# Kernel optimization log

Hardware: AMD Instinct MI355X
Metric: run time of the kernel (lower is better)

Reference implementation:

```python
import jax, jax.numpy as jnp
import numpy as np

NH = 8
QCH = 256
KCH = 256
VCH = 256


def setup_inputs() -> dict:
    key = jax.random.key(0)
    ks = jax.random.split(key, 6)
    B, C, H, W = 8, 512, 28, 28
    return {
        "inputs": jax.random.normal(ks[0], (B, C, H, W), jnp.float32),
        "inputs_st": jax.random.normal(ks[1], (B, C, H, W), jnp.float32),
        "Wq": jax.random.normal(ks[2], (QCH, C), jnp.float32) * 0.02,
        "bq": jnp.zeros((QCH,), jnp.float32),
        "Wkv": jax.random.normal(ks[3], (KCH + VCH, C), jnp.float32) * 0.02,
        "bkv": jnp.zeros((KCH + VCH,), jnp.float32),
        "Wo": jax.random.normal(ks[4], (512, VCH), jnp.float32) * 0.02,
        "bo": jnp.zeros((512,), jnp.float32),
    }


def reference(inputs, inputs_st, Wq, bq, Wkv, bkv, Wo, bo):
    B, C, H, W = inputs.shape
    dkh = KCH // NH  # scale uses k-channels per head, as in source

    # 1x1 conv projections == channel matmuls
    q = jnp.einsum('bchw,oc->bohw', inputs, Wq) + bq[None, :, None, None]
    kv = jnp.einsum('bchw,oc->bohw', inputs_st, Wkv) + bkv[None, :, None, None]
    k, v = kv[:, :KCH], kv[:, KCH:]

    # split heads: (B, Nh, ch//Nh, H, W)
    q = q.reshape(B, NH, QCH // NH, H, W) * (dkh ** -0.5)
    k = k.reshape(B, NH, KCH // NH, H, W)
    v = v.reshape(B, NH, VCH // NH, H, W)

    flat_q = q.reshape(B, NH, QCH // NH, H * W)
    flat_k = k.reshape(B, NH, KCH // NH, H * W)
    flat_v = v.reshape(B, NH, VCH // NH, H * W)

    # logits: (B, Nh, HqWq, HW) = q^T k
    logits = jnp.einsum('bnds,bndt->bnst', flat_q, flat_k)
    # NOTE: source applies softmax over dim=1 (the head axis), not the key axis
    weights = jax.nn.softmax(logits, axis=1)
    # attn_out: (B, Nh, HqWq, dvh)
    attn_out = jnp.einsum('bnst,bndt->bnsd', weights, flat_v)
    # faithful raw reshapes (no transpose), matching torch.reshape semantics
    attn_out = attn_out.reshape(B, NH, VCH // NH, H, W)
    attn_out = attn_out.reshape(B, VCH, H, W)

    out = jnp.einsum('bchw,oc->bohw', attn_out, Wo) + bo[None, :, None, None]
    return out
```

## Files before the change

### kernel.cpp

```cpp
#include <hip/hip_runtime.h>

#define SS 784
#define NQE 1605632

typedef float f32x4 __attribute__((ext_vector_type(4)));
typedef short s16x8 __attribute__((ext_vector_type(8)));

__device__ inline ushort f2bf(float f) {
    union { float f; unsigned u; } v; v.f = f;
    return (ushort)((v.u + 0x7fff + ((v.u >> 16) & 1)) >> 16);
}
__device__ inline float bf2f(ushort h) {
    union { unsigned u; float f; } v; v.u = ((unsigned)h) << 16;
    return v.f;
}
__device__ inline unsigned cvt_pk_bf16(float lo, float hi) {
    unsigned r;
    asm("v_cvt_pk_bf16_f32 %0, %1, %2" : "=v"(r) : "v"(lo), "v"(hi));
    return r;
}

__global__ __launch_bounds__(256) void transpose_cvt2(const float* __restrict__ X0,
                                                      const float* __restrict__ X1,
                                                      ushort* __restrict__ Xt0,
                                                      ushort* __restrict__ Xt1) {
    __shared__ ushort Ts[64][72];
    const int tid = threadIdx.x;
    const int p0 = blockIdx.x * 64, c0 = blockIdx.y * 64;
    const int z  = blockIdx.z;
    const int b  = z & 7;
    const float*  X  = (z < 8) ? X0 : X1;
    ushort*       Xt = (z < 8) ? Xt0 : Xt1;
    const int cr = tid >> 2, ch = (tid & 3) * 16;
    if (p0 + ch < SS) {
        const float* src = X + ((size_t)b * 512 + c0 + cr) * SS + p0 + ch;
        #pragma unroll
        for (int jj = 0; jj < 4; ++jj) {
            float4 v = *(const float4*)(src + jj * 4);
            Ts[ch + jj * 4 + 0][cr] = f2bf(v.x);
            Ts[ch + jj * 4 + 1][cr] = f2bf(v.y);
            Ts[ch + jj * 4 + 2][cr] = f2bf(v.z);
            Ts[ch + jj * 4 + 3][cr] = f2bf(v.w);
        }
    } else {
        #pragma unroll
        for (int j = 0; j < 16; ++j) Ts[ch + j][cr] = 0;
    }
    __syncthreads();
    const int pr = tid >> 2, cc = (tid & 3) * 16;
    if (p0 + pr < SS) {
        ushort* dst = Xt + ((size_t)b * SS + p0 + pr) * 512 + c0 + cc;
        *(s16x8*)dst       = *(const s16x8*)&Ts[pr][cc];
        *(s16x8*)(dst + 8) = *(const s16x8*)&Ts[pr][cc + 8];
    }
}

__global__ __launch_bounds__(256) void gemm_qkv(const ushort* __restrict__ xt_q,
                                                const ushort* __restrict__ xt_kv,
                                                const float* __restrict__ Wq,
                                                const float* __restrict__ bq,
                                                const float* __restrict__ Wkv,
                                                const float* __restrict__ bkv,
                                                ushort* __restrict__ qt,
                                                ushort* __restrict__ kt,
                                                ushort* __restrict__ vv,
                                                float qscale) {
    __shared__ ushort As[128 * 40];
    __shared__ ushort Bs[128 * 40];
    const int id  = blockIdx.x;
    const int b   = id & 7;
    const int sub = id >> 3;
    const int oy  = sub % 6;
    const int p0  = (sub / 6) * 128;
    const int mode = (oy < 2) ? 0 : (oy < 4 ? 1 : 2);
    const ushort* Xt  = (mode == 0) ? xt_q : xt_kv;
    const float* Wg   = (mode == 0) ? Wq : Wkv;
    const float* bias = (mode == 0) ? bq : bkv;
    const int o0w = (mode == 0) ? oy * 128 : (oy - 2) * 128;

    const int tid = threadIdx.x;
    const int lane = tid & 63, wave = tid >> 6;
    const int wm = wave >> 1, wn = wave & 1;
    const int lg = lane >> 4, lm = lane & 15;
    const int srow = tid >> 1, shalf = (tid & 1) * 16;

    const f32x4 Z4 = {0.f, 0.f, 0.f, 0.f};
    const s16x8 Z8 = {0, 0, 0, 0, 0, 0, 0, 0};
    f32x4 acc[4][4];
    #pragma unroll
    for (int m = 0; m < 4; ++m)
        #pragma unroll
        for (int n = 0; n < 4; ++n) acc[m][n] = Z4;

    for (int c0 = 0; c0 < 512; c0 += 32) {
        __syncthreads();
        {
            const float* src = Wg + (size_t)(o0w + srow) * 512 + c0 + shalf;
            ushort tmp[16];
            #pragma unroll
            for (int jj = 0; jj < 4; ++jj) {
                float4 v = *(const float4*)(src + jj * 4);
                tmp[jj * 4 + 0] = f2bf(v.x); tmp[jj * 4 + 1] = f2bf(v.y);
                tmp[jj * 4 + 2] = f2bf(v.z); tmp[jj * 4 + 3] = f2bf(v.w);
            }
            *(s16x8*)&As[srow * 40 + shalf]     = *(s16x8*)&tmp[0];
            *(s16x8*)&As[srow * 40 + shalf + 8] = *(s16x8*)&tmp[8];
        }
        {
            int p = p0 + srow;
            s16x8 v0 = Z8, v1 = Z8;
            if (p < SS) {
                const ushort* src = Xt + ((size_t)b * SS + p) * 512 + c0 + shalf;
                v0 = *(const s16x8*)src;
                v1 = *(const s16x8*)(src + 8);
            }
            *(s16x8*)&Bs[srow * 40 + shalf]     = v0;
            *(s16x8*)&Bs[srow * 40 + shalf + 8] = v1;
        }
        __syncthreads();
        s16x8 af[4], bf[4];
        #pragma unroll
        for (int m = 0; m < 4; ++m) af[m] = *(const s16x8*)&As[(wm * 64 + m * 16 + lm) * 40 + 8 * lg];
        #pragma unroll
        for (int n = 0; n < 4; ++n) bf[n] = *(const s16x8*)&Bs[(wn * 64 + n * 16 + lm) * 40 + 8 * lg];
        #pragma unroll
        for (int m = 0; m < 4; ++m)
            #pragma unroll
            for (int n = 0; n < 4; ++n)
                acc[m][n] = __builtin_amdgcn_mfma_f32_16x16x32_bf16(af[m], bf[n], acc[m][n], 0, 0, 0);
    }

    if (mode < 2) {
        ushort* outT = (mode == 0) ? qt : kt;
        const float scale = (mode == 0) ? qscale : 1.0f;
        #pragma unroll
        for (int m = 0; m < 4; ++m) {
            const int o = o0w + wm * 64 + m * 16 + 4 * lg;
            float bv[4];
            #pragma unroll
            for (int r = 0; r < 4; ++r) bv[r] = bias[o + r];
            #pragma unroll
            for (int n = 0; n < 4; ++n) {
                const int p = p0 + wn * 64 + n * 16 + lm;
                if (p < SS) {
                    ushort4 w;
                    w.x = f2bf((acc[m][n][0] + bv[0]) * scale);
                    w.y = f2bf((acc[m][n][1] + bv[1]) * scale);
                    w.z = f2bf((acc[m][n][2] + bv[2]) * scale);
                    w.w = f2bf((acc[m][n][3] + bv[3]) * scale);
                    *(ushort4*)&outT[((size_t)b * SS + p) * 256 + o] = w;
                }
            }
        }
    } else {
        #pragma unroll
        for (int m = 0; m < 4; ++m) {
            const int ob = o0w + wm * 64 + m * 16 + 4 * lg;
            float bv[4];
            #pragma unroll
            for (int r = 0; r < 4; ++r) bv[r] = bias[ob + r];
            #pragma unroll
            for (int n = 0; n < 4; ++n) {
                const int p = p0 + wn * 64 + n * 16 + lm;
                if (p < SS) {
                    #pragma unroll
                    for (int r = 0; r < 4; ++r) {
                        const int c = ob - 256 + r;
                        vv[((size_t)b * 256 + c) * SS + p] = f2bf(acc[m][n][r] + bv[r]);
                    }
                }
            }
        }
    }
}

#define KROW 280
#define VROW 40
#define PROW 40

__global__ __launch_bounds__(256, 3) void attn_mfma(const ushort* __restrict__ qt,
                                                    const ushort* __restrict__ kt,
                                                    const ushort* __restrict__ vv,
                                                    ushort* __restrict__ pb,
                                                    ushort* __restrict__ p4) {
    __shared__ ushort ks[32 * KROW];
    __shared__ ushort vs[256 * VROW];
    __shared__ ushort pls[4 * 2 * 16 * PROW];
    const int tid  = threadIdx.x;
    const int lane = tid & 63;
    const int wave = tid >> 6;
    const int b     = blockIdx.x;
    const int stile = blockIdx.y / 5;
    const int ts    = blockIdx.y % 5;
    int strip = stile * 4 + wave;
    const bool valid = (strip < 49);
    if (!valid) strip = 48;
    const int s0 = strip * 16;

    const int lg = lane >> 4, lm = lane & 15;
    const s16x8 Z8 = {0, 0, 0, 0, 0, 0, 0, 0};
    const f32x4 Z4 = {0.f, 0.f, 0.f, 0.f};

    s16x8 qf[8];
    const ushort* qbase = qt + ((size_t)b * SS + s0 + lm) * 256 + 8 * lg;
    #pragma unroll
    for (int n = 0; n < 8; ++n) qf[n] = *(const s16x8*)(qbase + n * 32);

    f32x4 oacc[8][2];
    #pragma unroll
    for (int n = 0; n < 8; ++n) { oacc[n][0] = Z4; oacc[n][1] = Z4; }

    const ushort* ktb = kt + (size_t)b * SS * 256;
    const ushort* vb  = vv + (size_t)b * 256 * SS;
    ushort* pbase = pls + wave * (2 * 16 * PROW);

    for (int ti = ts * 5; ti < ts * 5 + 5; ++ti) {
        const int t0 = ti * 32;
        __syncthreads();
        {
            const int row = tid >> 3, ce = (tid & 7) * 32;
            const int t = t0 + row;
            const ushort* src = ktb + (size_t)t * 256 + ce;
            #pragma unroll
            for (int j = 0; j < 4; ++j) {
                s16x8 v = (t < SS) ? *(const s16x8*)(src + 8 * j) : Z8;
                *(s16x8*)&ks[row * KROW + ce + 8 * j] = v;
            }
        }
        {
            const ushort* src = vb + (size_t)tid * SS + t0;
            #pragma unroll
            for (int j = 0; j < 4; ++j) {
                s16x8 v = (t0 + 8 * j < SS) ? *(const s16x8*)(src + 8 * j) : Z8;
                *(s16x8*)&vs[tid * VROW + 8 * j] = v;
            }
        }
        __syncthreads();

        unsigned pku[2][8][2];
        #pragma unroll
        for (int h = 0; h < 2; ++h) {
            f32x4 lacc[8];
            #pragma unroll
            for (int n = 0; n < 8; ++n) {
                s16x8 ak = *(const s16x8*)&ks[(h * 16 + lm) * KROW + n * 32 + 8 * lg];
                lacc[n] = __builtin_amdgcn_mfma_f32_16x16x32_bf16(ak, qf[n], Z4, 0, 0, 0);
            }
            #pragma unroll
            for (int r = 0; r < 4; ++r) {
                float e[8]; float sum = 0.f;
                #pragma unroll
                for (int n = 0; n < 8; ++n) { e[n] = exp2f(lacc[n][r]); sum += e[n]; }
                float inv;
                asm("v_rcp_f32 %0, %1" : "=v"(inv) : "v"(sum));
                #pragma unroll
                for (int n = 0; n < 8; ++n) lacc[n][r] = e[n] * inv;
            }
            #pragma unroll
            for (int n = 0; n < 8; ++n) {
                pku[h][n][0] = cvt_pk_bf16(lacc[n][0], lacc[n][1]);
                pku[h][n][1] = cvt_pk_bf16(lacc[n][2], lacc[n][3]);
            }
        }

        #pragma unroll
        for (int n = 0; n < 8; ++n) {
            ushort* pw = pbase + (n & 1) * (16 * PROW);
            uint2 w0; w0.x = pku[0][n][0]; w0.y = pku[0][n][1];
            *(uint2*)&pw[lm * PROW + 4 * lg] = w0;
            uint2 w1; w1.x = pku[1][n][0]; w1.y = pku[1][n][1];
            *(uint2*)&pw[lm * PROW + 16 + 4 * lg] = w1;
            s16x8 pbf = *(const s16x8*)&pw[lm * PROW + 8 * lg];
            #pragma unroll
            for (int dh = 0; dh < 2; ++dh) {
                s16x8 va = *(const s16x8*)&vs[(n * 32 + dh * 16 + lm) * VROW + 8 * lg];
                oacc[n][dh] = __builtin_amdgcn_mfma_f32_16x16x32_bf16(va, pbf, oacc[n][dh], 0, 0, 0);
            }
        }
    }

    if (valid) {
        ushort* part = (ts < 4) ? (pb + (size_t)ts * NQE) : p4;
        const size_t base = (size_t)b * 200704 + (size_t)s0 * 32 + lm * 32 + 4 * lg;
        #pragma unroll
        for (int n = 0; n < 8; ++n) {
            #pragma unroll
            for (int dh = 0; dh < 2; ++dh) {
                uint2 w;
                w.x = cvt_pk_bf16(oacc[n][dh][0], oacc[n][dh][1]);
                w.y = cvt_pk_bf16(oacc[n][dh][2], oacc[n][dh][3]);
                *(uint2*)&part[base + n * 25088 + dh * 16] = w;
            }
        }
    }
}

__global__ __launch_bounds__(256) void gemm_out5(const ushort* __restrict__ a0,
                                                 const ushort* __restrict__ a1,
                                                 const ushort* __restrict__ a2,
                                                 const ushort* __restrict__ a3,
                                                 const ushort* __restrict__ a4,
                                                 const float* __restrict__ Wg,
                                                 const float* __restrict__ bias,
                                                 float* __restrict__ outp) {
    __shared__ ushort As[128 * 40];
    __shared__ ushort Bs[128 * 40];
    const int tid = threadIdx.x;
    const int lane = tid & 63, wave = tid >> 6;
    const int wm = wave >> 1, wn = wave & 1;
    const int lg = lane >> 4, lm = lane & 15;
    const int b  = blockIdx.x;
    const int p0 = blockIdx.y * 128;
    const int o0 = blockIdx.z * 128;
    const int srow = tid >> 1, shalf = (tid & 1) * 16;
    const int tc = tid >> 3;
    const int tp = (tid & 7) * 16;

    const f32x4 Z4 = {0.f, 0.f, 0.f, 0.f};
    f32x4 acc[4][4];
    #pragma unroll
    for (int m = 0; m < 4; ++m)
        #pragma unroll
        for (int n = 0; n < 4; ++n) acc[m][n] = Z4;

    for (int c0 = 0; c0 < 256; c0 += 32) {
        __syncthreads();
        {
            const int p = p0 + tp;
            if (p < SS) {
                const size_t off = ((size_t)b * 256 + c0 + tc) * SS + p;
                #pragma unroll
                for (int jj = 0; jj < 2; ++jj) {
                    s16x8 v0 = *(const s16x8*)(a0 + off + 8 * jj);
                    s16x8 v1 = *(const s16x8*)(a1 + off + 8 * jj);
                    s16x8 v2 = *(const s16x8*)(a2 + off + 8 * jj);
                    s16x8 v3 = *(const s16x8*)(a3 + off + 8 * jj);
                    s16x8 v4 = *(const s16x8*)(a4 + off + 8 * jj);
                    #pragma unroll
                    for (int j = 0; j < 8; ++j) {
                        float s = bf2f((ushort)v0[j]) + bf2f((ushort)v1[j]) + bf2f((ushort)v2[j])
                                + bf2f((ushort)v3[j]) + bf2f((ushort)v4[j]);
                        As[(tp + jj * 8 + j) * 40 + tc] = f2bf(s);
                    }
                }
            } else {
                #pragma unroll
                for (int j = 0; j < 16; ++j) As[(tp + j) * 40 + tc] = 0;
            }
        }
        {
            const float* src = Wg + (size_t)(o0 + srow) * 256 + c0 + shalf;
            ushort tmp[16];
            #pragma unroll
            for (int jj = 0; jj < 4; ++jj) {
                float4 v = *(const float4*)(src + jj * 4);
                tmp[jj * 4 + 0] = f2bf(v.x); tmp[jj * 4 + 1] = f2bf(v.y);
                tmp[jj * 4 + 2] = f2bf(v.z); tmp[jj * 4 + 3] = f2bf(v.w);
            }
            *(s16x8*)&Bs[srow * 40 + shalf]     = *(s16x8*)&tmp[0];
            *(s16x8*)&Bs[srow * 40 + shalf + 8] = *(s16x8*)&tmp[8];
        }
        __syncthreads();
        s16x8 af[4], bf[4];
        #pragma unroll
        for (int m = 0; m < 4; ++m) af[m] = *(const s16x8*)&As[(wm * 64 + m * 16 + lm) * 40 + 8 * lg];
        #pragma unroll
        for (int n = 0; n < 4; ++n) bf[n] = *(const s16x8*)&Bs[(wn * 64 + n * 16 + lm) * 40 + 8 * lg];
        #pragma unroll
        for (int m = 0; m < 4; ++m)
            #pragma unroll
            for (int n = 0; n < 4; ++n)
                acc[m][n] = __builtin_amdgcn_mfma_f32_16x16x32_bf16(af[m], bf[n], acc[m][n], 0, 0, 0);
    }

    #pragma unroll
    for (int n = 0; n < 4; ++n) {
        const int o = o0 + wn * 64 + n * 16 + lm;
        const float bv = bias[o];
        #pragma unroll
        for (int m = 0; m < 4; ++m) {
            const int p = p0 + wm * 64 + m * 16 + 4 * lg;
            if (p < SS) {
                f32x4 v;
                #pragma unroll
                for (int r = 0; r < 4; ++r) v[r] = acc[m][n][r] + bv;
                *(f32x4*)&outp[((size_t)b * 512 + o) * SS + p] = v;
            }
        }
    }
}

extern "C" void kernel_launch(void* const* d_in, const int* in_sizes, int n_in,
                              void* d_out, int out_size, void* d_ws, size_t ws_size,
                              hipStream_t stream) {
    const float* inputs    = (const float*)d_in[0];
    const float* inputs_st = (const float*)d_in[1];
    const float* Wq        = (const float*)d_in[2];
    const float* bq        = (const float*)d_in[3];
    const float* Wkv       = (const float*)d_in[4];
    const float* bkv       = (const float*)d_in[5];
    const float* Wo        = (const float*)d_in[6];
    const float* bo        = (const float*)d_in[7];
    float* out = (float*)d_out;

    ushort* W     = (ushort*)d_ws;
    ushort* xt_q  = W;
    ushort* xt_kv = W + 2 * (size_t)NQE;
    ushort* qt    = W + 4 * (size_t)NQE;
    ushort* kt    = W + 5 * (size_t)NQE;
    ushort* vv    = W + 6 * (size_t)NQE;
    ushort* p4    = W + 7 * (size_t)NQE;

    const float qscale = (float)(1.4426950408889634 / 5.656854249492380195);

    transpose_cvt2<<<dim3(13, 8, 16), dim3(256), 0, stream>>>(inputs, inputs_st, xt_q, xt_kv);
    gemm_qkv<<<dim3(336), dim3(256), 0, stream>>>(xt_q, xt_kv, Wq, bq, Wkv, bkv, qt, kt, vv, qscale);
    attn_mfma<<<dim3(8, 65), dim3(256), 0, stream>>>(qt, kt, vv, W, p4);
    gemm_out5<<<dim3(8, 7, 4), dim3(256), 0, stream>>>(W, W + (size_t)NQE, W + 2 * (size_t)NQE,
                                                       W + 3 * (size_t)NQE, p4, Wo, bo, out);
}
```

Measured before the change: 91.84 us.

## Widen attention blocks to eight waves sharing each K/V tile

The attention kernel now runs 512 threads per block, with eight query strips per block instead of four, so every K/V tile staged in shared memory serves twice as many waves. The grid shrinks from 65 to 35 y-blocks and each thread loads half as much K/V data. The per-wave P scratch buffer drops from two alternating slots to one, which saves LDS but serialises reuse of that buffer across the n loop. The ragged last strip tile (49 strips) now leaves more invalid waves idle, and the launch bound of 512 threads with 6 waves per SIMD may restrict registers.

```diff
diff --git a/kernel.cpp b/kernel.cpp
--- a/kernel.cpp
+++ b/kernel.cpp
@@ -178,21 +178,21 @@
 #define VROW 40
 #define PROW 40
 
-__global__ __launch_bounds__(256, 3) void attn_mfma(const ushort* __restrict__ qt,
+__global__ __launch_bounds__(512, 6) void attn_mfma(const ushort* __restrict__ qt,
                                                     const ushort* __restrict__ kt,
                                                     const ushort* __restrict__ vv,
                                                     ushort* __restrict__ pb,
                                                     ushort* __restrict__ p4) {
     __shared__ ushort ks[32 * KROW];
     __shared__ ushort vs[256 * VROW];
-    __shared__ ushort pls[4 * 2 * 16 * PROW];
+    __shared__ ushort pls[8][16 * PROW];
     const int tid  = threadIdx.x;
     const int lane = tid & 63;
     const int wave = tid >> 6;
     const int b     = blockIdx.x;
     const int stile = blockIdx.y / 5;
     const int ts    = blockIdx.y % 5;
-    int strip = stile * 4 + wave;
+    int strip = stile * 8 + wave;
     const bool valid = (strip < 49);
     if (!valid) strip = 48;
     const int s0 = strip * 16;
@@ -212,28 +212,28 @@
 
     const ushort* ktb = kt + (size_t)b * SS * 256;
     const ushort* vb  = vv + (size_t)b * 256 * SS;
-    ushort* pbase = pls + wave * (2 * 16 * PROW);
+    ushort* pw = pls[wave];
+
+    const int krow = tid >> 4, kce = (tid & 15) * 16;
+    const int vc = tid >> 1, vtoff = (tid & 1) * 16;
 
     for (int ti = ts * 5; ti < ts * 5 + 5; ++ti) {
         const int t0 = ti * 32;
         __syncthreads();
         {
-            const int row = tid >> 3, ce = (tid & 7) * 32;
-            const int t = t0 + row;
-            const ushort* src = ktb + (size_t)t * 256 + ce;
-            #pragma unroll
-            for (int j = 0; j < 4; ++j) {
-                s16x8 v = (t < SS) ? *(const s16x8*)(src + 8 * j) : Z8;
-                *(s16x8*)&ks[row * KROW + ce + 8 * j] = v;
-            }
-        }
-        {
-            const ushort* src = vb + (size_t)tid * SS + t0;
-            #pragma unroll
-            for (int j = 0; j < 4; ++j) {
-                s16x8 v = (t0 + 8 * j < SS) ? *(const s16x8*)(src + 8 * j) : Z8;
-                *(s16x8*)&vs[tid * VROW + 8 * j] = v;
-            }
+            const int t = t0 + krow;
+            const ushort* src = ktb + (size_t)t * 256 + kce;
+            s16x8 v0 = Z8, v1 = Z8;
+            if (t < SS) { v0 = *(const s16x8*)src; v1 = *(const s16x8*)(src + 8); }
+            *(s16x8*)&ks[krow * KROW + kce]     = v0;
+            *(s16x8*)&ks[krow * KROW + kce + 8] = v1;
+        }
+        {
+            const ushort* src = vb + (size_t)vc * SS + t0 + vtoff;
+            s16x8 v0 = (t0 + vtoff < SS)     ? *(const s16x8*)src       : Z8;
+            s16x8 v1 = (t0 + vtoff + 8 < SS) ? *(const s16x8*)(src + 8) : Z8;
+            *(s16x8*)&vs[vc * VROW + vtoff]     = v0;
+            *(s16x8*)&vs[vc * VROW + vtoff + 8] = v1;
         }
         __syncthreads();
 
@@ -265,7 +265,6 @@
 
         #pragma unroll
         for (int n = 0; n < 8; ++n) {
-            ushort* pw = pbase + (n & 1) * (16 * PROW);
             uint2 w0; w0.x = pku[0][n][0]; w0.y = pku[0][n][1];
             *(uint2*)&pw[lm * PROW + 4 * lg] = w0;
             uint2 w1; w1.x = pku[1][n][0]; w1.y = pku[1][n][1];
@@ -415,7 +414,7 @@
 
     transpose_cvt2<<<dim3(13, 8, 16), dim3(256), 0, stream>>>(inputs, inputs_st, xt_q, xt_kv);
     gemm_qkv<<<dim3(336), dim3(256), 0, stream>>>(xt_q, xt_kv, Wq, bq, Wkv, bkv, qt, kt, vv, qscale);
-    attn_mfma<<<dim3(8, 65), dim3(256), 0, stream>>>(qt, kt, vv, W, p4);
+    attn_mfma<<<dim3(8, 35), dim3(512), 0, stream>>>(qt, kt, vv, W, p4);
     gemm_out5<<<dim3(8, 7, 4), dim3(256), 0, stream>>>(W, W + (size_t)NQE, W + 2 * (size_t)NQE,
                                                        W + 3 * (size_t)NQE, p4, Wo, bo, out);
 }
```

After: 184.3 us. 101% more time.
